# Optimization experiments

Measured on AMD Instinct MI355X. Metric: run time of the kernel, lower is better.

## Reference

```python
import jax, jax.numpy as jnp
import numpy as np

B, N, DIM = 4, 2048, 256
HEADS, CODEBOOK, HD = 4, 8192, 64  # HD = DIM // HEADS


def setup_inputs() -> dict:
    key = jax.random.key(0)
    k1, k2 = jax.random.split(key)
    x = jax.random.normal(k1, (B, N, DIM), dtype=jnp.float32)
    embed = jax.random.normal(k2, (HEADS, CODEBOOK, HD), dtype=jnp.float32)
    return {"x": x, "embed": embed}


def reference(x, embed):
    b, n, dim = x.shape
    h, c, d = embed.shape
    # 'b n (h d) -> h b n d' then pack to 'h (b n) d'
    flat = x.reshape(b, n, h, d).transpose(2, 0, 1, 3).reshape(h, b * n, d)
    x2 = jnp.sum(flat * flat, axis=-1)              # [h, bn]
    y2 = jnp.sum(embed * embed, axis=-1)            # [h, c]
    xy = jnp.einsum('hmd,hcd->hmc', flat, embed)    # [h, bn, c]
    sq = x2[:, :, None] + y2[:, None, :] - 2.0 * xy
    dist = -jnp.sqrt(jnp.maximum(sq, 0.0))          # clamp for fp safety
    embed_ind = jnp.argmax(dist, axis=-1)           # [h, bn]
    # gather codes per head
    quantize = jnp.take_along_axis(embed, embed_ind[:, :, None], axis=1)  # [h, bn, d]
    # 'h (b n) d -> b n (h d)'
    quantize = quantize.reshape(h, b, n, d).transpose(1, 2, 0, 3).reshape(b, n, h * d)
    # 'h (b n) -> b n h'
    embed_ind = embed_ind.reshape(h, b, n).transpose(1, 2, 0)
    return quantize, embed_ind
```

## Files before the change

### kernel.cpp

```cpp
#include <hip/hip_runtime.h>
#include <hip/hip_bf16.h>


#define HEADS    4
#define CODEBOOK 8192
#define HD       64
#define BQ       8192
#define QOFF     (4 * 2048 * 256)
#define NPART    4
#define CPART    (CODEBOOK / NPART)
#define SCODES   64
#define NSTAGE   (CPART / SCODES)

typedef __bf16 bf16x8 __attribute__((ext_vector_type(8)));
typedef float  f32x4  __attribute__((ext_vector_type(4)));

__device__ float g_pval[NPART][HEADS * BQ];
__device__ int   g_pidx[NPART][HEADS * BQ];

__device__ inline void split3(float f, __bf16& b0, __bf16& b1, __bf16& b2) {
    b0 = (__bf16)f;
    float r = f - (float)b0;
    b1 = (__bf16)r;
    r -= (float)b1;
    b2 = (__bf16)r;
}

__global__ __launch_bounds__(256, 2) void dist_kernel(const float* __restrict__ x,
                                                      const float* __restrict__ embed) {
    __shared__ __align__(16) __bf16 tile[2][3][SCODES * 64];
    __shared__ float y2s[CPART];

    const int bid  = blockIdx.x;
    const int part = bid & 3;
    const int qg   = (bid >> 2) & 31;
    const int h    = bid >> 7;
    const int t    = threadIdx.x;
    const int wave = t >> 6;
    const int lane = t & 63;
    const int col  = lane & 15;
    const int quad = lane >> 4;

    const int qbase = qg * 256 + wave * 64;
    const int cbase = part * CPART;

    bf16x8 a[4][3][2];
#pragma unroll
    for (int rt = 0; rt < 4; rt++) {
#pragma unroll
        for (int kh = 0; kh < 2; kh++) {
            const float* p = x + ((size_t)(qbase + rt * 16 + col) * 256 + h * 64 + kh * 32 + quad * 8);
#pragma unroll
            for (int j = 0; j < 8; j++) {
                __bf16 b0, b1, b2;
                split3(p[j], b0, b1, b2);
                a[rt][0][kh][j] = b0;
                a[rt][1][kh][j] = b1;
                a[rt][2][kh][j] = b2;
            }
        }
    }

    const float* esrc = embed + ((size_t)h * CODEBOOK + cbase) * HD + (size_t)t * 8;
    const int row  = t >> 3;
    const int gsw  = (t & 7) ^ (row & 7);
    const int ldA  = row * 64 + gsw * 8;
    const int ldB  = (row + 32) * 64 + gsw * 8;

    float bv[4][4]; int bc[4][4];
#pragma unroll
    for (int rt = 0; rt < 4; rt++)
#pragma unroll
        for (int r = 0; r < 4; r++) { bv[rt][r] = 3.4e38f; bc[rt][r] = 0; }

    float4 pfA0, pfA1, pfB0, pfB1;

    auto stage_write = [&](int buf, int stage) {
        float fA[8] = {pfA0.x, pfA0.y, pfA0.z, pfA0.w, pfA1.x, pfA1.y, pfA1.z, pfA1.w};
        float fB[8] = {pfB0.x, pfB0.y, pfB0.z, pfB0.w, pfB1.x, pfB1.y, pfB1.z, pfB1.w};
        bf16x8 vA0, vA1, vA2, vB0, vB1, vB2;
        float ssA = 0.f, ssB = 0.f;
#pragma unroll
        for (int j = 0; j < 8; j++) {
            __bf16 b0, b1, b2;
            split3(fA[j], b0, b1, b2);
            vA0[j] = b0; vA1[j] = b1; vA2[j] = b2;
            ssA = fmaf(fA[j], fA[j], ssA);
            split3(fB[j], b0, b1, b2);
            vB0[j] = b0; vB1[j] = b1; vB2[j] = b2;
            ssB = fmaf(fB[j], fB[j], ssB);
        }
        *reinterpret_cast<bf16x8*>(&tile[buf][0][ldA]) = vA0;
        *reinterpret_cast<bf16x8*>(&tile[buf][1][ldA]) = vA1;
        *reinterpret_cast<bf16x8*>(&tile[buf][2][ldA]) = vA2;
        *reinterpret_cast<bf16x8*>(&tile[buf][0][ldB]) = vB0;
        *reinterpret_cast<bf16x8*>(&tile[buf][1][ldB]) = vB1;
        *reinterpret_cast<bf16x8*>(&tile[buf][2][ldB]) = vB2;
#pragma unroll
        for (int off = 4; off >= 1; off >>= 1) {
            ssA += __shfl_xor(ssA, off, 8);
            ssB += __shfl_xor(ssB, off, 8);
        }
        if ((t & 7) == 0) {
            y2s[stage * SCODES + row]      = 0.5f * ssA;
            y2s[stage * SCODES + row + 32] = 0.5f * ssB;
        }
    };
    auto stage_load = [&](int stage) {
        const float* ps = esrc + (size_t)stage * (SCODES * HD);
        pfA0 = *reinterpret_cast<const float4*>(ps);
        pfA1 = *reinterpret_cast<const float4*>(ps + 4);
        pfB0 = *reinterpret_cast<const float4*>(ps + 32 * HD);
        pfB1 = *reinterpret_cast<const float4*>(ps + 32 * HD + 4);
    };

    stage_load(0);
    stage_write(0, 0);
    stage_load(1);
    __syncthreads();

    const int swbase = col & 7;

    for (int s = 0; s < NSTAGE; s++) {
        if (s + 1 < NSTAGE) stage_write((s + 1) & 1, s + 1);
        if (s + 2 < NSTAGE) stage_load(s + 2);

#pragma unroll
        for (int inner = 0; inner < 4; inner++) {
            const int rbase = (inner * 16 + col) * 64;
            bf16x8 b[3][2];
#pragma unroll
            for (int lvl = 0; lvl < 3; lvl++)
#pragma unroll
                for (int kh = 0; kh < 2; kh++)
                    b[lvl][kh] = *reinterpret_cast<const bf16x8*>(
                        &tile[s & 1][lvl][rbase + ((((kh << 2) | quad) ^ swbase) << 3)]);

            const int   c  = s * SCODES + inner * 16 + col;
            const float yc = y2s[c];
#pragma unroll
            for (int rt = 0; rt < 4; rt++) {
                f32x4 acc = {0.f, 0.f, 0.f, 0.f};
#pragma unroll
                for (int kh = 0; kh < 2; kh++) {
                    acc = __builtin_amdgcn_mfma_f32_16x16x32_bf16(a[rt][0][kh], b[0][kh], acc, 0, 0, 0);
                    acc = __builtin_amdgcn_mfma_f32_16x16x32_bf16(a[rt][0][kh], b[1][kh], acc, 0, 0, 0);
                    acc = __builtin_amdgcn_mfma_f32_16x16x32_bf16(a[rt][1][kh], b[0][kh], acc, 0, 0, 0);
                    acc = __builtin_amdgcn_mfma_f32_16x16x32_bf16(a[rt][0][kh], b[2][kh], acc, 0, 0, 0);
                    acc = __builtin_amdgcn_mfma_f32_16x16x32_bf16(a[rt][1][kh], b[1][kh], acc, 0, 0, 0);
                    acc = __builtin_amdgcn_mfma_f32_16x16x32_bf16(a[rt][2][kh], b[0][kh], acc, 0, 0, 0);
                }
#pragma unroll
                for (int r = 0; r < 4; r++) {
                    float sv = yc - acc[r];
                    if (sv < bv[rt][r]) { bv[rt][r] = sv; bc[rt][r] = c; }
                }
            }
        }
        __syncthreads();
    }

#pragma unroll
    for (int rt = 0; rt < 4; rt++) {
#pragma unroll
        for (int r = 0; r < 4; r++) {
            float v = bv[rt][r]; int c = bc[rt][r];
#pragma unroll
            for (int off = 8; off >= 1; off >>= 1) {
                float ov = __shfl_xor(v, off, 16); int oc = __shfl_xor(c, off, 16);
                if (ov < v || (ov == v && oc < c)) { v = ov; c = oc; }
            }
            if (col == 0) {
                int q = h * BQ + qbase + rt * 16 + quad * 4 + r;
                g_pval[part][q] = v; g_pidx[part][q] = cbase + c;
            }
        }
    }
}

__global__ __launch_bounds__(256) void merge_kernel(const float* __restrict__ embed,
                                                    float* __restrict__ out) {
    int id = blockIdx.x * 256 + threadIdx.x;
    int m = id >> 2;
    int h = id & 3;
    int q = h * BQ + m;

    float bv = g_pval[0][q]; int bc = g_pidx[0][q];
#pragma unroll
    for (int p = 1; p < NPART; p++) {
        float v = g_pval[p][q]; int c = g_pidx[p][q];
        if (v < bv || (v == bv && c < bc)) { bv = v; bc = c; }
    }

    out[QOFF + id] = (float)bc;

    int idx = bc & (CODEBOOK - 1);
    const float* src = embed + ((size_t)h * CODEBOOK + idx) * HD;
    float*       dst = out + (size_t)m * 256 + h * 64;
#pragma unroll
    for (int i = 0; i < 16; i++)
        *reinterpret_cast<float4*>(dst + i * 4) = *reinterpret_cast<const float4*>(src + i * 4);
}

extern "C" void kernel_launch(void* const* d_in, const int* in_sizes, int n_in,
                              void* d_out, int out_size, void* d_ws, size_t ws_size,
                              hipStream_t stream) {
    const float* x     = (const float*)d_in[0];
    const float* embed = (const float*)d_in[1];
    float*       out   = (float*)d_out;

    dist_kernel <<<512, 256, 0, stream>>>(x, embed);
    merge_kernel<<<128, 256, 0, stream>>>(embed, out);
}
```

Before: 219.7 us.

## Precompute bf16 split of codebook in prep kernel; fold y2 into MFMA accumulator

```diff
diff --git a/kernel.cpp b/kernel.cpp
--- a/kernel.cpp
+++ b/kernel.cpp
@@ -15,8 +15,12 @@
 typedef __bf16 bf16x8 __attribute__((ext_vector_type(8)));
 typedef float  f32x4  __attribute__((ext_vector_type(4)));
 
-__device__ float g_pval[NPART][HEADS * BQ];
-__device__ int   g_pidx[NPART][HEADS * BQ];
+__device__ __bf16 g_p0[HEADS * CODEBOOK * HD];
+__device__ __bf16 g_p1[HEADS * CODEBOOK * HD];
+__device__ __bf16 g_p2[HEADS * CODEBOOK * HD];
+__device__ float  g_y2n[HEADS * CODEBOOK];
+__device__ float  g_pval[NPART][HEADS * BQ];
+__device__ int    g_pidx[NPART][HEADS * BQ];
 
 __device__ inline void split3(float f, __bf16& b0, __bf16& b1, __bf16& b2) {
     b0 = (__bf16)f;
@@ -26,8 +30,30 @@
     b2 = (__bf16)r;
 }
 
-__global__ __launch_bounds__(256, 2) void dist_kernel(const float* __restrict__ x,
-                                                      const float* __restrict__ embed) {
+__global__ __launch_bounds__(256) void prep_kernel(const float* __restrict__ embed) {
+    int gid = blockIdx.x * 256 + threadIdx.x;
+    const float* p = embed + (size_t)gid * 8;
+    float4 u = *reinterpret_cast<const float4*>(p);
+    float4 w = *reinterpret_cast<const float4*>(p + 4);
+    float f[8] = {u.x, u.y, u.z, u.w, w.x, w.y, w.z, w.w};
+    bf16x8 v0, v1, v2;
+    float ss = 0.f;
+#pragma unroll
+    for (int j = 0; j < 8; j++) {
+        __bf16 b0, b1, b2;
+        split3(f[j], b0, b1, b2);
+        v0[j] = b0; v1[j] = b1; v2[j] = b2;
+        ss = fmaf(f[j], f[j], ss);
+    }
+    *reinterpret_cast<bf16x8*>(g_p0 + (size_t)gid * 8) = v0;
+    *reinterpret_cast<bf16x8*>(g_p1 + (size_t)gid * 8) = v1;
+    *reinterpret_cast<bf16x8*>(g_p2 + (size_t)gid * 8) = v2;
+#pragma unroll
+    for (int off = 4; off >= 1; off >>= 1) ss += __shfl_xor(ss, off, 8);
+    if ((threadIdx.x & 7) == 0) g_y2n[gid >> 3] = -0.5f * ss;
+}
+
+__global__ __launch_bounds__(256, 2) void dist_kernel(const float* __restrict__ x) {
     __shared__ __align__(16) __bf16 tile[2][3][SCODES * 64];
     __shared__ float y2s[CPART];
 
@@ -61,7 +87,13 @@
         }
     }
 
-    const float* esrc = embed + ((size_t)h * CODEBOOK + cbase) * HD + (size_t)t * 8;
+    {
+        const float* yg = g_y2n + h * CODEBOOK + cbase + t * 8;
+        *reinterpret_cast<float4*>(y2s + t * 8)     = *reinterpret_cast<const float4*>(yg);
+        *reinterpret_cast<float4*>(y2s + t * 8 + 4) = *reinterpret_cast<const float4*>(yg + 4);
+    }
+
+    const size_t pbase = ((size_t)h * CODEBOOK + cbase) * HD + (size_t)t * 8;
     const int row  = t >> 3;
     const int gsw  = (t & 7) ^ (row & 7);
     const int ldA  = row * 64 + gsw * 8;
@@ -71,58 +103,37 @@
 #pragma unroll
     for (int rt = 0; rt < 4; rt++)
 #pragma unroll
-        for (int r = 0; r < 4; r++) { bv[rt][r] = 3.4e38f; bc[rt][r] = 0; }
-
-    float4 pfA0, pfA1, pfB0, pfB1;
-
-    auto stage_write = [&](int buf, int stage) {
-        float fA[8] = {pfA0.x, pfA0.y, pfA0.z, pfA0.w, pfA1.x, pfA1.y, pfA1.z, pfA1.w};
-        float fB[8] = {pfB0.x, pfB0.y, pfB0.z, pfB0.w, pfB1.x, pfB1.y, pfB1.z, pfB1.w};
-        bf16x8 vA0, vA1, vA2, vB0, vB1, vB2;
-        float ssA = 0.f, ssB = 0.f;
-#pragma unroll
-        for (int j = 0; j < 8; j++) {
-            __bf16 b0, b1, b2;
-            split3(fA[j], b0, b1, b2);
-            vA0[j] = b0; vA1[j] = b1; vA2[j] = b2;
-            ssA = fmaf(fA[j], fA[j], ssA);
-            split3(fB[j], b0, b1, b2);
-            vB0[j] = b0; vB1[j] = b1; vB2[j] = b2;
-            ssB = fmaf(fB[j], fB[j], ssB);
-        }
-        *reinterpret_cast<bf16x8*>(&tile[buf][0][ldA]) = vA0;
-        *reinterpret_cast<bf16x8*>(&tile[buf][1][ldA]) = vA1;
-        *reinterpret_cast<bf16x8*>(&tile[buf][2][ldA]) = vA2;
-        *reinterpret_cast<bf16x8*>(&tile[buf][0][ldB]) = vB0;
-        *reinterpret_cast<bf16x8*>(&tile[buf][1][ldB]) = vB1;
-        *reinterpret_cast<bf16x8*>(&tile[buf][2][ldB]) = vB2;
-#pragma unroll
-        for (int off = 4; off >= 1; off >>= 1) {
-            ssA += __shfl_xor(ssA, off, 8);
-            ssB += __shfl_xor(ssB, off, 8);
-        }
-        if ((t & 7) == 0) {
-            y2s[stage * SCODES + row]      = 0.5f * ssA;
-            y2s[stage * SCODES + row + 32] = 0.5f * ssB;
-        }
+        for (int r = 0; r < 4; r++) { bv[rt][r] = -3.4e38f; bc[rt][r] = 0; }
+
+    bf16x8 pf[6];
+
+    auto stage_load = [&](int stage) {
+        const size_t o = pbase + (size_t)stage * (SCODES * HD);
+        pf[0] = *reinterpret_cast<const bf16x8*>(g_p0 + o);
+        pf[1] = *reinterpret_cast<const bf16x8*>(g_p1 + o);
+        pf[2] = *reinterpret_cast<const bf16x8*>(g_p2 + o);
+        pf[3] = *reinterpret_cast<const bf16x8*>(g_p0 + o + 32 * HD);
+        pf[4] = *reinterpret_cast<const bf16x8*>(g_p1 + o + 32 * HD);
+        pf[5] = *reinterpret_cast<const bf16x8*>(g_p2 + o + 32 * HD);
     };
-    auto stage_load = [&](int stage) {
-        const float* ps = esrc + (size_t)stage * (SCODES * HD);
-        pfA0 = *reinterpret_cast<const float4*>(ps);
-        pfA1 = *reinterpret_cast<const float4*>(ps + 4);
-        pfB0 = *reinterpret_cast<const float4*>(ps + 32 * HD);
-        pfB1 = *reinterpret_cast<const float4*>(ps + 32 * HD + 4);
+    auto stage_write = [&](int buf) {
+        *reinterpret_cast<bf16x8*>(&tile[buf][0][ldA]) = pf[0];
+        *reinterpret_cast<bf16x8*>(&tile[buf][1][ldA]) = pf[1];
+        *reinterpret_cast<bf16x8*>(&tile[buf][2][ldA]) = pf[2];
+        *reinterpret_cast<bf16x8*>(&tile[buf][0][ldB]) = pf[3];
+        *reinterpret_cast<bf16x8*>(&tile[buf][1][ldB]) = pf[4];
+        *reinterpret_cast<bf16x8*>(&tile[buf][2][ldB]) = pf[5];
     };
 
     stage_load(0);
-    stage_write(0, 0);
+    stage_write(0);
     stage_load(1);
     __syncthreads();
 
     const int swbase = col & 7;
 
     for (int s = 0; s < NSTAGE; s++) {
-        if (s + 1 < NSTAGE) stage_write((s + 1) & 1, s + 1);
+        if (s + 1 < NSTAGE) stage_write((s + 1) & 1);
         if (s + 2 < NSTAGE) stage_load(s + 2);
 
 #pragma unroll
@@ -136,24 +147,25 @@
                     b[lvl][kh] = *reinterpret_cast<const bf16x8*>(
                         &tile[s & 1][lvl][rbase + ((((kh << 2) | quad) ^ swbase) << 3)]);
 
-            const int   c  = s * SCODES + inner * 16 + col;
-            const float yc = y2s[c];
+            const int   c   = s * SCODES + inner * 16 + col;
+            const float ycn = y2s[c];
 #pragma unroll
             for (int rt = 0; rt < 4; rt++) {
-                f32x4 acc = {0.f, 0.f, 0.f, 0.f};
+                f32x4 aA = {ycn, ycn, ycn, ycn};
+                f32x4 aB = {0.f, 0.f, 0.f, 0.f};
 #pragma unroll
                 for (int kh = 0; kh < 2; kh++) {
-                    acc = __builtin_amdgcn_mfma_f32_16x16x32_bf16(a[rt][0][kh], b[0][kh], acc, 0, 0, 0);
-                    acc = __builtin_amdgcn_mfma_f32_16x16x32_bf16(a[rt][0][kh], b[1][kh], acc, 0, 0, 0);
-                    acc = __builtin_amdgcn_mfma_f32_16x16x32_bf16(a[rt][1][kh], b[0][kh], acc, 0, 0, 0);
-                    acc = __builtin_amdgcn_mfma_f32_16x16x32_bf16(a[rt][0][kh], b[2][kh], acc, 0, 0, 0);
-                    acc = __builtin_amdgcn_mfma_f32_16x16x32_bf16(a[rt][1][kh], b[1][kh], acc, 0, 0, 0);
-                    acc = __builtin_amdgcn_mfma_f32_16x16x32_bf16(a[rt][2][kh], b[0][kh], acc, 0, 0, 0);
+                    aA = __builtin_amdgcn_mfma_f32_16x16x32_bf16(a[rt][0][kh], b[0][kh], aA, 0, 0, 0);
+                    aB = __builtin_amdgcn_mfma_f32_16x16x32_bf16(a[rt][0][kh], b[1][kh], aB, 0, 0, 0);
+                    aA = __builtin_amdgcn_mfma_f32_16x16x32_bf16(a[rt][1][kh], b[1][kh], aA, 0, 0, 0);
+                    aB = __builtin_amdgcn_mfma_f32_16x16x32_bf16(a[rt][1][kh], b[0][kh], aB, 0, 0, 0);
+                    aA = __builtin_amdgcn_mfma_f32_16x16x32_bf16(a[rt][0][kh], b[2][kh], aA, 0, 0, 0);
+                    aB = __builtin_amdgcn_mfma_f32_16x16x32_bf16(a[rt][2][kh], b[0][kh], aB, 0, 0, 0);
                 }
+                f32x4 acc = aA + aB;
 #pragma unroll
                 for (int r = 0; r < 4; r++) {
-                    float sv = yc - acc[r];
-                    if (sv < bv[rt][r]) { bv[rt][r] = sv; bc[rt][r] = c; }
+                    if (acc[r] > bv[rt][r]) { bv[rt][r] = acc[r]; bc[rt][r] = c; }
                 }
             }
         }
@@ -168,7 +180,7 @@
 #pragma unroll
             for (int off = 8; off >= 1; off >>= 1) {
                 float ov = __shfl_xor(v, off, 16); int oc = __shfl_xor(c, off, 16);
-                if (ov < v || (ov == v && oc < c)) { v = ov; c = oc; }
+                if (ov > v || (ov == v && oc < c)) { v = ov; c = oc; }
             }
             if (col == 0) {
                 int q = h * BQ + qbase + rt * 16 + quad * 4 + r;
@@ -189,7 +201,7 @@
 #pragma unroll
     for (int p = 1; p < NPART; p++) {
         float v = g_pval[p][q]; int c = g_pidx[p][q];
-        if (v < bv || (v == bv && c < bc)) { bv = v; bc = c; }
+        if (v > bv || (v == bv && c < bc)) { bv = v; bc = c; }
     }
 
     out[QOFF + id] = (float)bc;
@@ -209,6 +221,7 @@
     const float* embed = (const float*)d_in[1];
     float*       out   = (float*)d_out;
 
-    dist_kernel <<<512, 256, 0, stream>>>(x, embed);
-    merge_kernel<<<128, 256, 0, stream>>>(embed, out);
-}
+    prep_kernel <<<1024, 256, 0, stream>>>(embed);
+    dist_kernel <<<512,  256, 0, stream>>>(x);
+    merge_kernel<<<128,  256, 0, stream>>>(embed, out);
+}
```

Measured after the change: 229.7 us. 1.05x slower.

## Replace 3-way bf16 split with scaled 2-way fp16 split and double codebook partitions

Applied to the files above, without the earlier changes.

```diff
diff --git a/kernel.cpp b/kernel.cpp
--- a/kernel.cpp
+++ b/kernel.cpp
@@ -7,34 +7,34 @@
 #define HD       64
 #define BQ       8192
 #define QOFF     (4 * 2048 * 256)
-#define NPART    4
+#define NPART    8
 #define CPART    (CODEBOOK / NPART)
 #define SCODES   64
 #define NSTAGE   (CPART / SCODES)
-
-typedef __bf16 bf16x8 __attribute__((ext_vector_type(8)));
-typedef float  f32x4  __attribute__((ext_vector_type(4)));
+#define RSCALE   4096.0f
+#define RINV     (1.0f / 4096.0f)
+
+typedef _Float16 f16x8 __attribute__((ext_vector_type(8)));
+typedef float    f32x4 __attribute__((ext_vector_type(4)));
 
 __device__ float g_pval[NPART][HEADS * BQ];
 __device__ int   g_pidx[NPART][HEADS * BQ];
 
-__device__ inline void split3(float f, __bf16& b0, __bf16& b1, __bf16& b2) {
-    b0 = (__bf16)f;
-    float r = f - (float)b0;
-    b1 = (__bf16)r;
-    r -= (float)b1;
-    b2 = (__bf16)r;
+__device__ inline void split2(float f, _Float16& h0, _Float16& h1) {
+    h0 = (_Float16)f;
+    float r = f - (float)h0;
+    h1 = (_Float16)(r * RSCALE);
 }
 
 __global__ __launch_bounds__(256, 2) void dist_kernel(const float* __restrict__ x,
                                                       const float* __restrict__ embed) {
-    __shared__ __align__(16) __bf16 tile[2][3][SCODES * 64];
+    __shared__ __align__(16) _Float16 tile[2][2][SCODES * 64];
     __shared__ float y2s[CPART];
 
     const int bid  = blockIdx.x;
-    const int part = bid & 3;
-    const int qg   = (bid >> 2) & 31;
-    const int h    = bid >> 7;
+    const int part = bid & 7;
+    const int qg   = (bid >> 3) & 31;
+    const int h    = bid >> 8;
     const int t    = threadIdx.x;
     const int wave = t >> 6;
     const int lane = t & 63;
@@ -44,7 +44,7 @@
     const int qbase = qg * 256 + wave * 64;
     const int cbase = part * CPART;
 
-    bf16x8 a[4][3][2];
+    f16x8 a[4][2][2];
 #pragma unroll
     for (int rt = 0; rt < 4; rt++) {
 #pragma unroll
@@ -52,11 +52,10 @@
             const float* p = x + ((size_t)(qbase + rt * 16 + col) * 256 + h * 64 + kh * 32 + quad * 8);
 #pragma unroll
             for (int j = 0; j < 8; j++) {
-                __bf16 b0, b1, b2;
-                split3(p[j], b0, b1, b2);
-                a[rt][0][kh][j] = b0;
-                a[rt][1][kh][j] = b1;
-                a[rt][2][kh][j] = b2;
+                _Float16 h0, h1;
+                split2(p[j], h0, h1);
+                a[rt][0][kh][j] = h0;
+                a[rt][1][kh][j] = h1;
             }
         }
     }
@@ -71,39 +70,37 @@
 #pragma unroll
     for (int rt = 0; rt < 4; rt++)
 #pragma unroll
-        for (int r = 0; r < 4; r++) { bv[rt][r] = 3.4e38f; bc[rt][r] = 0; }
+        for (int r = 0; r < 4; r++) { bv[rt][r] = -3.4e38f; bc[rt][r] = 0; }
 
     float4 pfA0, pfA1, pfB0, pfB1;
 
     auto stage_write = [&](int buf, int stage) {
         float fA[8] = {pfA0.x, pfA0.y, pfA0.z, pfA0.w, pfA1.x, pfA1.y, pfA1.z, pfA1.w};
         float fB[8] = {pfB0.x, pfB0.y, pfB0.z, pfB0.w, pfB1.x, pfB1.y, pfB1.z, pfB1.w};
-        bf16x8 vA0, vA1, vA2, vB0, vB1, vB2;
+        f16x8 vA0, vA1, vB0, vB1;
         float ssA = 0.f, ssB = 0.f;
 #pragma unroll
         for (int j = 0; j < 8; j++) {
-            __bf16 b0, b1, b2;
-            split3(fA[j], b0, b1, b2);
-            vA0[j] = b0; vA1[j] = b1; vA2[j] = b2;
+            _Float16 h0, h1;
+            split2(fA[j], h0, h1);
+            vA0[j] = h0; vA1[j] = h1;
             ssA = fmaf(fA[j], fA[j], ssA);
-            split3(fB[j], b0, b1, b2);
-            vB0[j] = b0; vB1[j] = b1; vB2[j] = b2;
+            split2(fB[j], h0, h1);
+            vB0[j] = h0; vB1[j] = h1;
             ssB = fmaf(fB[j], fB[j], ssB);
         }
-        *reinterpret_cast<bf16x8*>(&tile[buf][0][ldA]) = vA0;
-        *reinterpret_cast<bf16x8*>(&tile[buf][1][ldA]) = vA1;
-        *reinterpret_cast<bf16x8*>(&tile[buf][2][ldA]) = vA2;
-        *reinterpret_cast<bf16x8*>(&tile[buf][0][ldB]) = vB0;
-        *reinterpret_cast<bf16x8*>(&tile[buf][1][ldB]) = vB1;
-        *reinterpret_cast<bf16x8*>(&tile[buf][2][ldB]) = vB2;
+        *reinterpret_cast<f16x8*>(&tile[buf][0][ldA]) = vA0;
+        *reinterpret_cast<f16x8*>(&tile[buf][1][ldA]) = vA1;
+        *reinterpret_cast<f16x8*>(&tile[buf][0][ldB]) = vB0;
+        *reinterpret_cast<f16x8*>(&tile[buf][1][ldB]) = vB1;
 #pragma unroll
         for (int off = 4; off >= 1; off >>= 1) {
             ssA += __shfl_xor(ssA, off, 8);
             ssB += __shfl_xor(ssB, off, 8);
         }
         if ((t & 7) == 0) {
-            y2s[stage * SCODES + row]      = 0.5f * ssA;
-            y2s[stage * SCODES + row + 32] = 0.5f * ssB;
+            y2s[stage * SCODES + row]      = -0.5f * ssA;
+            y2s[stage * SCODES + row + 32] = -0.5f * ssB;
         }
     };
     auto stage_load = [&](int stage) {
@@ -128,32 +125,30 @@
 #pragma unroll
         for (int inner = 0; inner < 4; inner++) {
             const int rbase = (inner * 16 + col) * 64;
-            bf16x8 b[3][2];
-#pragma unroll
-            for (int lvl = 0; lvl < 3; lvl++)
+            f16x8 b[2][2];
+#pragma unroll
+            for (int lvl = 0; lvl < 2; lvl++)
 #pragma unroll
                 for (int kh = 0; kh < 2; kh++)
-                    b[lvl][kh] = *reinterpret_cast<const bf16x8*>(
+                    b[lvl][kh] = *reinterpret_cast<const f16x8*>(
                         &tile[s & 1][lvl][rbase + ((((kh << 2) | quad) ^ swbase) << 3)]);
 
-            const int   c  = s * SCODES + inner * 16 + col;
-            const float yc = y2s[c];
+            const int   c   = s * SCODES + inner * 16 + col;
+            const float ycn = y2s[c];
 #pragma unroll
             for (int rt = 0; rt < 4; rt++) {
-                f32x4 acc = {0.f, 0.f, 0.f, 0.f};
+                f32x4 aA = {ycn, ycn, ycn, ycn};
+                f32x4 aB = {0.f, 0.f, 0.f, 0.f};
 #pragma unroll
                 for (int kh = 0; kh < 2; kh++) {
-                    acc = __builtin_amdgcn_mfma_f32_16x16x32_bf16(a[rt][0][kh], b[0][kh], acc, 0, 0, 0);
-                    acc = __builtin_amdgcn_mfma_f32_16x16x32_bf16(a[rt][0][kh], b[1][kh], acc, 0, 0, 0);
-                    acc = __builtin_amdgcn_mfma_f32_16x16x32_bf16(a[rt][1][kh], b[0][kh], acc, 0, 0, 0);
-                    acc = __builtin_amdgcn_mfma_f32_16x16x32_bf16(a[rt][0][kh], b[2][kh], acc, 0, 0, 0);
-                    acc = __builtin_amdgcn_mfma_f32_16x16x32_bf16(a[rt][1][kh], b[1][kh], acc, 0, 0, 0);
-                    acc = __builtin_amdgcn_mfma_f32_16x16x32_bf16(a[rt][2][kh], b[0][kh], acc, 0, 0, 0);
+                    aA = __builtin_amdgcn_mfma_f32_16x16x32_f16(a[rt][0][kh], b[0][kh], aA, 0, 0, 0);
+                    aB = __builtin_amdgcn_mfma_f32_16x16x32_f16(a[rt][0][kh], b[1][kh], aB, 0, 0, 0);
+                    aB = __builtin_amdgcn_mfma_f32_16x16x32_f16(a[rt][1][kh], b[0][kh], aB, 0, 0, 0);
                 }
 #pragma unroll
                 for (int r = 0; r < 4; r++) {
-                    float sv = yc - acc[r];
-                    if (sv < bv[rt][r]) { bv[rt][r] = sv; bc[rt][r] = c; }
+                    float sv = fmaf(aB[r], RINV, aA[r]);
+                    if (sv > bv[rt][r]) { bv[rt][r] = sv; bc[rt][r] = c; }
                 }
             }
         }
@@ -168,7 +163,7 @@
 #pragma unroll
             for (int off = 8; off >= 1; off >>= 1) {
                 float ov = __shfl_xor(v, off, 16); int oc = __shfl_xor(c, off, 16);
-                if (ov < v || (ov == v && oc < c)) { v = ov; c = oc; }
+                if (ov > v || (ov == v && oc < c)) { v = ov; c = oc; }
             }
             if (col == 0) {
                 int q = h * BQ + qbase + rt * 16 + quad * 4 + r;
@@ -189,7 +184,7 @@
 #pragma unroll
     for (int p = 1; p < NPART; p++) {
         float v = g_pval[p][q]; int c = g_pidx[p][q];
-        if (v < bv || (v == bv && c < bc)) { bv = v; bc = c; }
+        if (v > bv || (v == bv && c < bc)) { bv = v; bc = c; }
     }
 
     out[QOFF + id] = (float)bc;
@@ -209,6 +204,6 @@
     const float* embed = (const float*)d_in[1];
     float*       out   = (float*)d_out;
 
-    dist_kernel <<<512, 256, 0, stream>>>(x, embed);
-    merge_kernel<<<128, 256, 0, stream>>>(embed, out);
-}
+    dist_kernel <<<1024, 256, 0, stream>>>(x, embed);
+    merge_kernel<<<128,  256, 0, stream>>>(embed, out);
+}
```

Result: faster. 189.5 us (-13.7%).
